# Kernel tuning notes

Hardware: AMD Instinct MI355X
Metric: run time of the kernel (lower is better)

## Reference

```python
import jax, jax.numpy as jnp
import numpy as np

DIM = 4096
NUM_HEAD = 32
NUM_KV_HEAD = 8
ROPE_THETA = 10000.0
B, T = 2, 2048


def apply_rope(x, start_pos=0, theta=ROPE_THETA):
    # x: [B, T, H, d_head]; rotate half-split pairs by position-dependent angles
    d = x.shape[-1]
    half = d // 2
    inv_freq = 1.0 / (theta ** (jnp.arange(0, half, dtype=jnp.float32) / half))
    pos = jnp.arange(x.shape[1], dtype=jnp.float32) + start_pos  # [T]
    ang = pos[:, None] * inv_freq[None, :]                       # [T, half]
    cos = jnp.cos(ang)[None, :, None, :]
    sin = jnp.sin(ang)[None, :, None, :]
    x1, x2 = x[..., :half], x[..., half:]
    return jnp.concatenate([x1 * cos - x2 * sin, x1 * sin + x2 * cos], axis=-1)


def setup_inputs() -> dict:
    key = jax.random.key(0)
    ks = jax.random.split(key, 5)
    scale = 0.02
    X = jax.random.normal(ks[0], (B, T, DIM), dtype=jnp.float32)
    Wq = jax.random.normal(ks[1], (DIM, DIM), dtype=jnp.float32) * scale
    Wk = jax.random.normal(ks[2], (DIM, DIM // NUM_HEAD * NUM_KV_HEAD), dtype=jnp.float32) * scale
    Wv = jax.random.normal(ks[3], (DIM, DIM // NUM_HEAD * NUM_KV_HEAD), dtype=jnp.float32) * scale
    Wo = jax.random.normal(ks[4], (DIM, DIM), dtype=jnp.float32) * scale
    return {"X": X, "Wq": Wq, "Wk": Wk, "Wv": Wv, "Wo": Wo}


def reference(X, Wq, Wk, Wv, Wo):
    Bs, Ts, C = X.shape
    H, Hkv = NUM_HEAD, NUM_KV_HEAD
    dh = C // H
    G = H // Hkv  # GQA group size

    Q = apply_rope((X @ Wq).reshape(Bs, Ts, H, dh))      # [B,T,H,dh]
    K = apply_rope((X @ Wk).reshape(Bs, Ts, Hkv, dh))    # [B,T,Hkv,dh]
    V = (X @ Wv).reshape(Bs, Ts, Hkv, dh)                # [B,T,Hkv,dh]

    # [B,Hkv,G,T,dh]: grouped layout equivalent to repeat_interleave on head dim
    Qh = Q.transpose(0, 2, 1, 3).reshape(Bs, Hkv, G, Ts, dh)
    Kh = K.transpose(0, 2, 1, 3)  # [B,Hkv,T,dh]
    Vh = V.transpose(0, 2, 1, 3)

    scores = jnp.einsum('bkgtd,bksd->bkgts', Qh, Kh) / jnp.sqrt(jnp.float32(dh))
    causal = jnp.tril(jnp.ones((Ts, Ts), dtype=bool))
    scores = jnp.where(causal[None, None, None], scores, -jnp.inf)
    attn = jax.nn.softmax(scores, axis=-1)
    out = jnp.einsum('bkgts,bksd->bkgtd', attn, Vh)       # [B,Hkv,G,T,dh]
    out = out.reshape(Bs, H, Ts, dh).transpose(0, 2, 1, 3).reshape(Bs, Ts, C)
    return out @ Wo
```

## Files before the change

kernel.cpp:

```cpp
#include <hip/hip_runtime.h>
#include <hip/hip_bf16.h>
#include <cstdint>
#include <cstddef>

#define B_   2
#define T_   2048
#define DIM_ 4096
#define H_   32
#define HKV_ 8
#define DH_  128
#define MROWS (B_*T_)

typedef __bf16 bf16_t;
typedef bf16_t bf16x8 __attribute__((ext_vector_type(8)));
typedef bf16_t bf16x4 __attribute__((ext_vector_type(4)));
typedef float  f32x4  __attribute__((ext_vector_type(4)));

typedef __attribute__((address_space(1))) void gvoid_t;
typedef __attribute__((address_space(3))) void lvoid_t;

__device__ __forceinline__ void gld_lds16(const void* g, void* l) {
  __builtin_amdgcn_global_load_lds((gvoid_t*)g, (lvoid_t*)l, 16, 0, 0);
}

__device__ __forceinline__ f32x4 mfma16(bf16x8 a, bf16x8 b, f32x4 c) {
  return __builtin_amdgcn_mfma_f32_16x16x32_bf16(a, b, c, 0, 0, 0);
}

__global__ void cast_f32_bf16(const float* __restrict__ in,
                              bf16_t* __restrict__ out, int n4) {
  int i = blockIdx.x * blockDim.x + threadIdx.x;
  if (i < n4) {
    float4 v = ((const float4*)in)[i];
    bf16x4 o;
    o[0] = (bf16_t)v.x; o[1] = (bf16_t)v.y; o[2] = (bf16_t)v.z; o[3] = (bf16_t)v.w;
    ((bf16x4*)out)[i] = o;
  }
}

__global__ void transpose_cast(const float* __restrict__ in,
                               bf16_t* __restrict__ out, int K, int N) {
  __shared__ float tile[32][33];
  int n0 = blockIdx.x * 32, k0 = blockIdx.y * 32;
  int tx = threadIdx.x, ty = threadIdx.y;
#pragma unroll
  for (int j = 0; j < 4; ++j)
    tile[ty + j*8][tx] = in[(size_t)(k0 + ty + j*8) * N + n0 + tx];
  __syncthreads();
#pragma unroll
  for (int j = 0; j < 4; ++j)
    out[(size_t)(n0 + ty + j*8) * K + k0 + tx] = (bf16_t)tile[tx][ty + j*8];
}

template <int OUT_F32>
__global__ __launch_bounds__(256, 2)
void gemm_bt(const bf16_t* __restrict__ A, const bf16_t* __restrict__ BT,
             void* __restrict__ C, int M, int N, int K) {
  __shared__ __align__(16) bf16_t Als[128 * 32];
  __shared__ __align__(16) bf16_t Bls[128 * 32];
  const int tid  = threadIdx.x;
  const int wave = tid >> 6, lane = tid & 63;
  const int quad = lane >> 4, l16 = lane & 15;
  const int wm = wave >> 1, wn = wave & 1;
  const int m0 = blockIdx.y * 128, n0 = blockIdx.x * 128;

  f32x4 acc[4][4] = {};

  const int srow = lane >> 2;
  const int scol = (lane & 3) * 8;

  for (int k0 = 0; k0 < K; k0 += 32) {
#pragma unroll
    for (int c = 0; c < 2; ++c) {
      int ch = wave * 2 + c;
      gld_lds16(A + (size_t)(m0 + ch*16 + srow) * K + k0 + scol,
                &Als[ch*512 + srow*32 + scol]);
    }
#pragma unroll
    for (int c = 0; c < 2; ++c) {
      int ch = wave * 2 + c;
      gld_lds16(BT + (size_t)(n0 + ch*16 + srow) * K + k0 + scol,
                &Bls[ch*512 + srow*32 + scol]);
    }
    __syncthreads();

    bf16x8 af[4], bfr[4];
#pragma unroll
    for (int mi = 0; mi < 4; ++mi)
      af[mi] = *(const bf16x8*)&Als[(wm*64 + mi*16 + l16)*32 + quad*8];
#pragma unroll
    for (int ni = 0; ni < 4; ++ni)
      bfr[ni] = *(const bf16x8*)&Bls[(wn*64 + ni*16 + l16)*32 + quad*8];
#pragma unroll
    for (int mi = 0; mi < 4; ++mi)
#pragma unroll
      for (int ni = 0; ni < 4; ++ni)
        acc[mi][ni] = mfma16(af[mi], bfr[ni], acc[mi][ni]);
    __syncthreads();
  }

#pragma unroll
  for (int mi = 0; mi < 4; ++mi)
#pragma unroll
    for (int ni = 0; ni < 4; ++ni)
#pragma unroll
      for (int r = 0; r < 4; ++r) {
        int row = m0 + wm*64 + mi*16 + quad*4 + r;
        int col = n0 + wn*64 + ni*16 + l16;
        if (OUT_F32)
          ((float*)C)[(size_t)row * N + col] = acc[mi][ni][r];
        else
          ((bf16_t*)C)[(size_t)row * N + col] = (bf16_t)acc[mi][ni][r];
      }
}

__global__ void rope_kernel(bf16_t* __restrict__ X, int Hn, int total) {
  int i = blockIdx.x * blockDim.x + threadIdx.x;
  if (i >= total) return;
  int d   = i & 63;
  int rem = i >> 6;
  int h   = rem % Hn; rem /= Hn;
  int t   = rem % T_;
  int b   = rem / T_;
  size_t base = ((size_t)(b * T_ + t) * Hn + h) * DH_;
  float x1 = (float)X[base + d];
  float x2 = (float)X[base + 64 + d];
  float inv_freq = expf(-(float)d * 0.14391156758f);
  float ang = (float)t * inv_freq;
  float s, c;
  sincosf(ang, &s, &c);
  X[base + d]      = (bf16_t)(x1 * c - x2 * s);
  X[base + 64 + d] = (bf16_t)(x1 * s + x2 * c);
}

__global__ void v_transpose(const bf16_t* __restrict__ Vb,
                            bf16_t* __restrict__ VT) {
  __shared__ bf16_t tile[32][33];
  int t0 = blockIdx.x * 32;
  int d0 = blockIdx.y * 32;
  int bk = blockIdx.z;
  int b = bk >> 3, kv = bk & 7;
  int tx = threadIdx.x, ty = threadIdx.y;
#pragma unroll
  for (int j = 0; j < 4; ++j)
    tile[ty + j*8][tx] =
        Vb[(size_t)(b * T_ + t0 + ty + j*8) * (HKV_*DH_) + kv*DH_ + d0 + tx];
  __syncthreads();
#pragma unroll
  for (int j = 0; j < 4; ++j)
    VT[((size_t)bk * DH_ + d0 + ty + j*8) * T_ + t0 + tx] = tile[tx][ty + j*8];
}

__global__ __launch_bounds__(256, 2)
void flash_attn(const bf16_t* __restrict__ Qb, const bf16_t* __restrict__ Kb,
                const bf16_t* __restrict__ VT, bf16_t* __restrict__ Ob) {
  __shared__ __align__(16) bf16_t Pls[128 * 72];

  const int tid = threadIdx.x, wave = tid >> 6, lane = tid & 63;
  const int quad = lane >> 4, l16 = lane & 15;

  const int linear = blockIdx.x;
  const int xcd  = linear & 7;
  const int slot = linear >> 3;
  const int g    = ((slot >> 6) << 3) + xcd;
  const int b    = g >> 3, kv = g & 7;
  const int j    = slot & 63;
  const int qt   = 15 - (j >> 2);
  const int h    = kv * 4 + (j & 3);

  bf16x8 q[2][4];
#pragma unroll
  for (int mi = 0; mi < 2; ++mi) {
    const bf16_t* base =
        Qb + (size_t)(b*T_ + qt*128 + wave*32 + mi*16 + l16) * DIM_ + h*DH_;
#pragma unroll
    for (int kk = 0; kk < 4; ++kk)
      q[mi][kk] = *(const bf16x8*)(base + kk*32 + quad*8);
  }

  float m_st[2][4], l_st[2][4];
  f32x4 o_acc[2][8] = {};
#pragma unroll
  for (int mi = 0; mi < 2; ++mi)
#pragma unroll
    for (int r = 0; r < 4; ++r) { m_st[mi][r] = -1e30f; l_st[mi][r] = 0.f; }

  const int nkv = 2 * (qt + 1);
  const float S2 = 0.08838834764831845f * 1.4426950408889634f;
  const float THRraw = 8.0f / 0.08838834764831845f;

  const bf16_t* Kbase = Kb + (size_t)b * T_ * (HKV_*DH_) + kv * DH_;
  const bf16_t* Vbase = VT + (size_t)(b*HKV_ + kv) * DH_ * T_;

  for (int kvt = 0; kvt < nkv; ++kvt) {
    f32x4 s[2][4] = {};
#pragma unroll
    for (int kk = 0; kk < 4; ++kk) {
      bf16x8 kf[4];
#pragma unroll
      for (int ni = 0; ni < 4; ++ni) {
        int krow = kvt*64 + ni*16 + l16;
        kf[ni] = *(const bf16x8*)(Kbase + (size_t)krow * (HKV_*DH_) + kk*32 + quad*8);
      }
      __builtin_amdgcn_s_setprio(1);
#pragma unroll
      for (int mi = 0; mi < 2; ++mi)
#pragma unroll
        for (int ni = 0; ni < 4; ++ni)
          s[mi][ni] = mfma16(q[mi][kk], kf[ni], s[mi][ni]);
      __builtin_amdgcn_s_setprio(0);
    }

    const bool need_mask = (kvt >= 2*qt);
#pragma unroll
    for (int mi = 0; mi < 2; ++mi) {
      float mx[4];
#pragma unroll
      for (int r = 0; r < 4; ++r) {
        int rpos = qt*128 + wave*32 + mi*16 + quad*4 + r;
        float m = -1e30f;
#pragma unroll
        for (int ni = 0; ni < 4; ++ni) {
          float v = s[mi][ni][r];
          if (need_mask) {
            int cpos = kvt*64 + ni*16 + l16;
            if (cpos > rpos) v = -1e30f;
          }
          s[mi][ni][r] = v;
          m = fmaxf(m, v);
        }
#pragma unroll
        for (int off = 1; off < 16; off <<= 1)
          m = fmaxf(m, __shfl_xor(m, off, 64));
        mx[r] = m;
      }
      bool defer = true;
#pragma unroll
      for (int r = 0; r < 4; ++r)
        defer = defer && (mx[r] <= m_st[mi][r] + THRraw);
      if (__all(defer)) {
#pragma unroll
        for (int r = 0; r < 4; ++r) {
          float mn2 = m_st[mi][r] * S2;
          float rs = 0.f;
#pragma unroll
          for (int ni = 0; ni < 4; ++ni) {
            float pv = __builtin_amdgcn_exp2f(fmaf(s[mi][ni][r], S2, -mn2));
            s[mi][ni][r] = pv;
            rs += pv;
          }
#pragma unroll
          for (int off = 1; off < 16; off <<= 1)
            rs += __shfl_xor(rs, off, 64);
          l_st[mi][r] += rs;
        }
      } else {
        float al[4];
#pragma unroll
        for (int r = 0; r < 4; ++r) {
          float mnew = fmaxf(m_st[mi][r], mx[r]);
          al[r] = __builtin_amdgcn_exp2f((m_st[mi][r] - mnew) * S2);
          m_st[mi][r] = mnew;
          float mn2 = mnew * S2;
          float rs = 0.f;
#pragma unroll
          for (int ni = 0; ni < 4; ++ni) {
            float pv = __builtin_amdgcn_exp2f(fmaf(s[mi][ni][r], S2, -mn2));
            s[mi][ni][r] = pv;
            rs += pv;
          }
#pragma unroll
          for (int off = 1; off < 16; off <<= 1)
            rs += __shfl_xor(rs, off, 64);
          l_st[mi][r] = l_st[mi][r] * al[r] + rs;
        }
#pragma unroll
        for (int ni = 0; ni < 8; ++ni)
#pragma unroll
          for (int r = 0; r < 4; ++r) o_acc[mi][ni][r] *= al[r];
      }
#pragma unroll
      for (int ni = 0; ni < 4; ++ni)
#pragma unroll
        for (int r = 0; r < 4; ++r) {
          int prow = wave*32 + mi*16 + quad*4 + r;
          Pls[prow*72 + ni*16 + l16] = (bf16_t)s[mi][ni][r];
        }
    }

    bf16x8 pf[2][2];
#pragma unroll
    for (int kk = 0; kk < 2; ++kk)
#pragma unroll
      for (int mi = 0; mi < 2; ++mi)
        pf[kk][mi] = *(const bf16x8*)&Pls[(wave*32 + mi*16 + l16)*72 + kk*32 + quad*8];
#pragma unroll
    for (int ni = 0; ni < 8; ++ni) {
      int drow = ni*16 + l16;
      const bf16_t* vb = Vbase + (size_t)drow * T_ + kvt*64;
      bf16x8 va = *(const bf16x8*)(vb + quad*8);
      bf16x8 vc = *(const bf16x8*)(vb + 32 + quad*8);
      __builtin_amdgcn_s_setprio(1);
      o_acc[0][ni] = mfma16(pf[0][0], va, o_acc[0][ni]);
      o_acc[1][ni] = mfma16(pf[0][1], va, o_acc[1][ni]);
      o_acc[0][ni] = mfma16(pf[1][0], vc, o_acc[0][ni]);
      o_acc[1][ni] = mfma16(pf[1][1], vc, o_acc[1][ni]);
      __builtin_amdgcn_s_setprio(0);
    }
  }

#pragma unroll
  for (int mi = 0; mi < 2; ++mi) {
    float inv[4];
#pragma unroll
    for (int r = 0; r < 4; ++r) inv[r] = 1.f / l_st[mi][r];
#pragma unroll
    for (int ni = 0; ni < 8; ++ni)
#pragma unroll
      for (int r = 0; r < 4; ++r) {
        size_t row = (size_t)(b*T_ + qt*128 + wave*32 + mi*16 + quad*4 + r);
        int col = h*DH_ + ni*16 + l16;
        Ob[row * DIM_ + col] = (bf16_t)(o_acc[mi][ni][r] * inv[r]);
      }
  }
}

extern "C" void kernel_launch(void* const* d_in, const int* in_sizes, int n_in,
                              void* d_out, int out_size, void* d_ws, size_t ws_size,
                              hipStream_t stream) {
  const float* X  = (const float*)d_in[0];
  const float* Wq = (const float*)d_in[1];
  const float* Wk = (const float*)d_in[2];
  const float* Wv = (const float*)d_in[3];
  const float* Wo = (const float*)d_in[4];
  float* out = (float*)d_out;

  char* ws = (char*)d_ws;
  const size_t SZ_X  = (size_t)MROWS * DIM_ * 2;
  const size_t SZ_WQ = (size_t)DIM_ * DIM_ * 2;
  const size_t SZ_WK = (size_t)DIM_ * 1024 * 2;
  bf16_t* Xb  = (bf16_t*)(ws);
  bf16_t* WqT = (bf16_t*)(ws + SZ_X);
  bf16_t* WkT = (bf16_t*)(ws + SZ_X + SZ_WQ);
  bf16_t* WvT = (bf16_t*)(ws + SZ_X + SZ_WQ + SZ_WK);
  bf16_t* WoT = (bf16_t*)(ws + SZ_X + SZ_WQ + 2*SZ_WK);
  bf16_t* Qb  = (bf16_t*)(ws + SZ_X + 2*SZ_WQ + 2*SZ_WK);
  bf16_t* Kb  = (bf16_t*)(ws + 2*SZ_X + 2*SZ_WQ + 2*SZ_WK);
  bf16_t* Vb  = (bf16_t*)(ws + 2*SZ_X + 2*SZ_WQ + 3*SZ_WK);
  bf16_t* VT  = (bf16_t*)(ws + 2*SZ_X + 2*SZ_WQ + 4*SZ_WK);
  bf16_t* Ob  = Xb;

  {
    int n4 = MROWS * DIM_ / 4;
    cast_f32_bf16<<<(n4 + 255)/256, 256, 0, stream>>>(X, Xb, n4);
  }
  transpose_cast<<<dim3(DIM_/32, DIM_/32), dim3(32,8), 0, stream>>>(Wq, WqT, DIM_, DIM_);
  transpose_cast<<<dim3(1024/32, DIM_/32), dim3(32,8), 0, stream>>>(Wk, WkT, DIM_, 1024);
  transpose_cast<<<dim3(1024/32, DIM_/32), dim3(32,8), 0, stream>>>(Wv, WvT, DIM_, 1024);
  transpose_cast<<<dim3(DIM_/32, DIM_/32), dim3(32,8), 0, stream>>>(Wo, WoT, DIM_, DIM_);

  gemm_bt<0><<<dim3(DIM_/128, MROWS/128), 256, 0, stream>>>(Xb, WqT, Qb, MROWS, DIM_, DIM_);
  gemm_bt<0><<<dim3(1024/128, MROWS/128), 256, 0, stream>>>(Xb, WkT, Kb, MROWS, 1024, DIM_);
  gemm_bt<0><<<dim3(1024/128, MROWS/128), 256, 0, stream>>>(Xb, WvT, Vb, MROWS, 1024, DIM_);

  {
    int totq = B_ * T_ * H_ * 64;
    rope_kernel<<<(totq + 255)/256, 256, 0, stream>>>(Qb, H_, totq);
    int totk = B_ * T_ * HKV_ * 64;
    rope_kernel<<<(totk + 255)/256, 256, 0, stream>>>(Kb, HKV_, totk);
  }

  v_transpose<<<dim3(T_/32, DH_/32, B_*HKV_), dim3(32,8), 0, stream>>>(Vb, VT);

  flash_attn<<<dim3((T_/128) * H_ * B_), 256, 0, stream>>>(Qb, Kb, VT, Ob);

  gemm_bt<1><<<dim3(DIM_/128, MROWS/128), 256, 0, stream>>>(Ob, WoT, out, MROWS, DIM_, DIM_);
}
```

Baseline: 989.3 us.

## Fuse QKV projections into one GEMM and compute softmax row sums via MFMA

The three Q, K and V projection GEMMs become a single GEMM writing an interleaved QKV buffer with row stride 6144. This relies on WqT, WkT and WvT being contiguous in the workspace. RoPE, the V transpose and attention are updated to read through the new stride. In flash attention, the per-tile row-max shuffle reduction is skipped on the deferred path. The softmax denominator is now accumulated by MFMA against a vector of ones instead of shuffle reductions, which removes cross-lane work but makes the sum come from bf16-rounded probabilities.

```diff
diff --git a/kernel.cpp b/kernel.cpp
--- a/kernel.cpp
+++ b/kernel.cpp
@@ -10,6 +10,7 @@
 #define HKV_ 8
 #define DH_  128
 #define MROWS (B_*T_)
+#define QKV_LD 6144
 
 typedef __bf16 bf16_t;
 typedef bf16_t bf16x8 __attribute__((ext_vector_type(8)));
@@ -114,7 +115,7 @@
       }
 }
 
-__global__ void rope_kernel(bf16_t* __restrict__ X, int Hn, int total) {
+__global__ void rope_kernel(bf16_t* __restrict__ X, int Hn, int ld, int total) {
   int i = blockIdx.x * blockDim.x + threadIdx.x;
   if (i >= total) return;
   int d   = i & 63;
@@ -122,7 +123,7 @@
   int h   = rem % Hn; rem /= Hn;
   int t   = rem % T_;
   int b   = rem / T_;
-  size_t base = ((size_t)(b * T_ + t) * Hn + h) * DH_;
+  size_t base = (size_t)(b * T_ + t) * ld + h * DH_;
   float x1 = (float)X[base + d];
   float x2 = (float)X[base + 64 + d];
   float inv_freq = expf(-(float)d * 0.14391156758f);
@@ -134,7 +135,7 @@
 }
 
 __global__ void v_transpose(const bf16_t* __restrict__ Vb,
-                            bf16_t* __restrict__ VT) {
+                            bf16_t* __restrict__ VT, int ld) {
   __shared__ bf16_t tile[32][33];
   int t0 = blockIdx.x * 32;
   int d0 = blockIdx.y * 32;
@@ -144,7 +145,7 @@
 #pragma unroll
   for (int j = 0; j < 4; ++j)
     tile[ty + j*8][tx] =
-        Vb[(size_t)(b * T_ + t0 + ty + j*8) * (HKV_*DH_) + kv*DH_ + d0 + tx];
+        Vb[(size_t)(b * T_ + t0 + ty + j*8) * ld + kv*DH_ + d0 + tx];
   __syncthreads();
 #pragma unroll
   for (int j = 0; j < 4; ++j)
@@ -152,8 +153,8 @@
 }
 
 __global__ __launch_bounds__(256, 2)
-void flash_attn(const bf16_t* __restrict__ Qb, const bf16_t* __restrict__ Kb,
-                const bf16_t* __restrict__ VT, bf16_t* __restrict__ Ob) {
+void flash_attn(const bf16_t* __restrict__ QKV, const bf16_t* __restrict__ VT,
+                bf16_t* __restrict__ Ob) {
   __shared__ __align__(16) bf16_t Pls[128 * 72];
 
   const int tid = threadIdx.x, wave = tid >> 6, lane = tid & 63;
@@ -172,25 +173,30 @@
 #pragma unroll
   for (int mi = 0; mi < 2; ++mi) {
     const bf16_t* base =
-        Qb + (size_t)(b*T_ + qt*128 + wave*32 + mi*16 + l16) * DIM_ + h*DH_;
+        QKV + (size_t)(b*T_ + qt*128 + wave*32 + mi*16 + l16) * QKV_LD + h*DH_;
 #pragma unroll
     for (int kk = 0; kk < 4; ++kk)
       q[mi][kk] = *(const bf16x8*)(base + kk*32 + quad*8);
   }
 
-  float m_st[2][4], l_st[2][4];
+  float m_st[2][4];
   f32x4 o_acc[2][8] = {};
+  f32x4 l_acc[2] = {};
 #pragma unroll
   for (int mi = 0; mi < 2; ++mi)
 #pragma unroll
-    for (int r = 0; r < 4; ++r) { m_st[mi][r] = -1e30f; l_st[mi][r] = 0.f; }
+    for (int r = 0; r < 4; ++r) m_st[mi][r] = -1e30f;
 
   const int nkv = 2 * (qt + 1);
   const float S2 = 0.08838834764831845f * 1.4426950408889634f;
   const float THRraw = 8.0f / 0.08838834764831845f;
 
-  const bf16_t* Kbase = Kb + (size_t)b * T_ * (HKV_*DH_) + kv * DH_;
+  const bf16_t* Kbase = QKV + DIM_ + (size_t)b * T_ * QKV_LD + kv * DH_;
   const bf16_t* Vbase = VT + (size_t)(b*HKV_ + kv) * DH_ * T_;
+
+  bf16x8 vones;
+#pragma unroll
+  for (int i = 0; i < 8; ++i) vones[i] = (bf16_t)1.0f;
 
   for (int kvt = 0; kvt < nkv; ++kvt) {
     f32x4 s[2][4] = {};
@@ -200,7 +206,7 @@
 #pragma unroll
       for (int ni = 0; ni < 4; ++ni) {
         int krow = kvt*64 + ni*16 + l16;
-        kf[ni] = *(const bf16x8*)(Kbase + (size_t)krow * (HKV_*DH_) + kk*32 + quad*8);
+        kf[ni] = *(const bf16x8*)(Kbase + (size_t)krow * QKV_LD + kk*32 + quad*8);
       }
       __builtin_amdgcn_s_setprio(1);
 #pragma unroll
@@ -214,7 +220,7 @@
     const bool need_mask = (kvt >= 2*qt);
 #pragma unroll
     for (int mi = 0; mi < 2; ++mi) {
-      float mx[4];
+      float lmax[4];
 #pragma unroll
       for (int r = 0; r < 4; ++r) {
         int rpos = qt*128 + wave*32 + mi*16 + quad*4 + r;
@@ -229,63 +235,41 @@
           s[mi][ni][r] = v;
           m = fmaxf(m, v);
         }
-#pragma unroll
-        for (int off = 1; off < 16; off <<= 1)
-          m = fmaxf(m, __shfl_xor(m, off, 64));
-        mx[r] = m;
-      }
-      bool defer = true;
-#pragma unroll
-      for (int r = 0; r < 4; ++r)
-        defer = defer && (mx[r] <= m_st[mi][r] + THRraw);
-      if (__all(defer)) {
+        lmax[r] = m;
+      }
+      bool defer = (lmax[0] <= m_st[mi][0] + THRraw) &
+                   (lmax[1] <= m_st[mi][1] + THRraw) &
+                   (lmax[2] <= m_st[mi][2] + THRraw) &
+                   (lmax[3] <= m_st[mi][3] + THRraw);
+      if (!__all(defer)) {
+        float al[4];
 #pragma unroll
         for (int r = 0; r < 4; ++r) {
-          float mn2 = m_st[mi][r] * S2;
-          float rs = 0.f;
-#pragma unroll
-          for (int ni = 0; ni < 4; ++ni) {
-            float pv = __builtin_amdgcn_exp2f(fmaf(s[mi][ni][r], S2, -mn2));
-            s[mi][ni][r] = pv;
-            rs += pv;
-          }
+          float m = lmax[r];
 #pragma unroll
           for (int off = 1; off < 16; off <<= 1)
-            rs += __shfl_xor(rs, off, 64);
-          l_st[mi][r] += rs;
-        }
-      } else {
-        float al[4];
-#pragma unroll
-        for (int r = 0; r < 4; ++r) {
-          float mnew = fmaxf(m_st[mi][r], mx[r]);
+            m = fmaxf(m, __shfl_xor(m, off, 64));
+          float mnew = fmaxf(m_st[mi][r], m);
           al[r] = __builtin_amdgcn_exp2f((m_st[mi][r] - mnew) * S2);
           m_st[mi][r] = mnew;
-          float mn2 = mnew * S2;
-          float rs = 0.f;
-#pragma unroll
-          for (int ni = 0; ni < 4; ++ni) {
-            float pv = __builtin_amdgcn_exp2f(fmaf(s[mi][ni][r], S2, -mn2));
-            s[mi][ni][r] = pv;
-            rs += pv;
-          }
-#pragma unroll
-          for (int off = 1; off < 16; off <<= 1)
-            rs += __shfl_xor(rs, off, 64);
-          l_st[mi][r] = l_st[mi][r] * al[r] + rs;
         }
 #pragma unroll
         for (int ni = 0; ni < 8; ++ni)
 #pragma unroll
           for (int r = 0; r < 4; ++r) o_acc[mi][ni][r] *= al[r];
-      }
-#pragma unroll
-      for (int ni = 0; ni < 4; ++ni)
-#pragma unroll
-        for (int r = 0; r < 4; ++r) {
-          int prow = wave*32 + mi*16 + quad*4 + r;
-          Pls[prow*72 + ni*16 + l16] = (bf16_t)s[mi][ni][r];
+#pragma unroll
+        for (int r = 0; r < 4; ++r) l_acc[mi][r] *= al[r];
+      }
+#pragma unroll
+      for (int r = 0; r < 4; ++r) {
+        float mn2 = m_st[mi][r] * S2;
+        int prow = wave*32 + mi*16 + quad*4 + r;
+#pragma unroll
+        for (int ni = 0; ni < 4; ++ni) {
+          float pv = __builtin_amdgcn_exp2f(fmaf(s[mi][ni][r], S2, -mn2));
+          Pls[prow*72 + ni*16 + l16] = (bf16_t)pv;
         }
+      }
     }
 
     bf16x8 pf[2][2];
@@ -294,6 +278,14 @@
 #pragma unroll
       for (int mi = 0; mi < 2; ++mi)
         pf[kk][mi] = *(const bf16x8*)&Pls[(wave*32 + mi*16 + l16)*72 + kk*32 + quad*8];
+
+    __builtin_amdgcn_s_setprio(1);
+    l_acc[0] = mfma16(pf[0][0], vones, l_acc[0]);
+    l_acc[1] = mfma16(pf[0][1], vones, l_acc[1]);
+    l_acc[0] = mfma16(pf[1][0], vones, l_acc[0]);
+    l_acc[1] = mfma16(pf[1][1], vones, l_acc[1]);
+    __builtin_amdgcn_s_setprio(0);
+
 #pragma unroll
     for (int ni = 0; ni < 8; ++ni) {
       int drow = ni*16 + l16;
@@ -313,7 +305,7 @@
   for (int mi = 0; mi < 2; ++mi) {
     float inv[4];
 #pragma unroll
-    for (int r = 0; r < 4; ++r) inv[r] = 1.f / l_st[mi][r];
+    for (int r = 0; r < 4; ++r) inv[r] = 1.f / l_acc[mi][r];
 #pragma unroll
     for (int ni = 0; ni < 8; ++ni)
 #pragma unroll
@@ -336,18 +328,17 @@
   float* out = (float*)d_out;
 
   char* ws = (char*)d_ws;
-  const size_t SZ_X  = (size_t)MROWS * DIM_ * 2;
-  const size_t SZ_WQ = (size_t)DIM_ * DIM_ * 2;
-  const size_t SZ_WK = (size_t)DIM_ * 1024 * 2;
+  const size_t SZ_X   = (size_t)MROWS * DIM_ * 2;
+  const size_t SZ_WQ  = (size_t)DIM_ * DIM_ * 2;
+  const size_t SZ_WK  = (size_t)DIM_ * 1024 * 2;
+  const size_t SZ_QKV = (size_t)MROWS * QKV_LD * 2;
   bf16_t* Xb  = (bf16_t*)(ws);
   bf16_t* WqT = (bf16_t*)(ws + SZ_X);
   bf16_t* WkT = (bf16_t*)(ws + SZ_X + SZ_WQ);
   bf16_t* WvT = (bf16_t*)(ws + SZ_X + SZ_WQ + SZ_WK);
   bf16_t* WoT = (bf16_t*)(ws + SZ_X + SZ_WQ + 2*SZ_WK);
-  bf16_t* Qb  = (bf16_t*)(ws + SZ_X + 2*SZ_WQ + 2*SZ_WK);
-  bf16_t* Kb  = (bf16_t*)(ws + 2*SZ_X + 2*SZ_WQ + 2*SZ_WK);
-  bf16_t* Vb  = (bf16_t*)(ws + 2*SZ_X + 2*SZ_WQ + 3*SZ_WK);
-  bf16_t* VT  = (bf16_t*)(ws + 2*SZ_X + 2*SZ_WQ + 4*SZ_WK);
+  bf16_t* QKV = (bf16_t*)(ws + SZ_X + 2*SZ_WQ + 2*SZ_WK);
+  bf16_t* VT  = (bf16_t*)(ws + SZ_X + 2*SZ_WQ + 2*SZ_WK + SZ_QKV);
   bf16_t* Ob  = Xb;
 
   {
@@ -359,20 +350,18 @@
   transpose_cast<<<dim3(1024/32, DIM_/32), dim3(32,8), 0, stream>>>(Wv, WvT, DIM_, 1024);
   transpose_cast<<<dim3(DIM_/32, DIM_/32), dim3(32,8), 0, stream>>>(Wo, WoT, DIM_, DIM_);
 
-  gemm_bt<0><<<dim3(DIM_/128, MROWS/128), 256, 0, stream>>>(Xb, WqT, Qb, MROWS, DIM_, DIM_);
-  gemm_bt<0><<<dim3(1024/128, MROWS/128), 256, 0, stream>>>(Xb, WkT, Kb, MROWS, 1024, DIM_);
-  gemm_bt<0><<<dim3(1024/128, MROWS/128), 256, 0, stream>>>(Xb, WvT, Vb, MROWS, 1024, DIM_);
+  gemm_bt<0><<<dim3(QKV_LD/128, MROWS/128), 256, 0, stream>>>(Xb, WqT, QKV, MROWS, QKV_LD, DIM_);
 
   {
     int totq = B_ * T_ * H_ * 64;
-    rope_kernel<<<(totq + 255)/256, 256, 0, stream>>>(Qb, H_, totq);
+    rope_kernel<<<(totq + 255)/256, 256, 0, stream>>>(QKV, H_, QKV_LD, totq);
     int totk = B_ * T_ * HKV_ * 64;
-    rope_kernel<<<(totk + 255)/256, 256, 0, stream>>>(Kb, HKV_, totk);
-  }
-
-  v_transpose<<<dim3(T_/32, DH_/32, B_*HKV_), dim3(32,8), 0, stream>>>(Vb, VT);
-
-  flash_attn<<<dim3((T_/128) * H_ * B_), 256, 0, stream>>>(Qb, Kb, VT, Ob);
+    rope_kernel<<<(totk + 255)/256, 256, 0, stream>>>(QKV + DIM_, HKV_, QKV_LD, totk);
+  }
+
+  v_transpose<<<dim3(T_/32, DH_/32, B_*HKV_), dim3(32,8), 0, stream>>>(QKV + DIM_ + 1024, VT, QKV_LD);
+
+  flash_attn<<<dim3((T_/128) * H_ * B_), 256, 0, stream>>>(QKV, VT, Ob);
 
   gemm_bt<1><<<dim3(DIM_/128, MROWS/128), 256, 0, stream>>>(Ob, WoT, out, MROWS, DIM_, DIM_);
 }
```

Result: faster. 901.3 us (-8.9%).
